# Kernel tuning notes

Hardware: AMD Instinct MI355X
Metric: run time of the kernel (lower is better)

The kernel has to match this reference:

```python
import jax, jax.numpy as jnp
import numpy as np

N_NODES = 50000
N_EDGES = 600000
D = 128


def setup_inputs() -> dict:
    key = jax.random.key(0)
    k1, k2, k3, k4 = jax.random.split(key, 4)
    x = jax.random.normal(k1, (N_NODES, D), dtype=jnp.float32)
    edge_index = jax.random.randint(k2, (2, N_EDGES), 0, N_NODES, dtype=jnp.int64)
    # GCNConv linear weight (glorot-ish scale) and bias
    W = jax.random.normal(k3, (D, D), dtype=jnp.float32) * (1.0 / np.sqrt(D))
    b = jax.random.normal(k4, (D,), dtype=jnp.float32) * 0.01
    return {"x": x, "edge_index": edge_index, "W": W, "b": b}


def reference(x, edge_index, W, b):
    """ResGCN: x + GCNConv(x, edge_index).

    GCNConv (PyG defaults): add self-loops, symmetric deg^{-1/2} normalization,
    messages x_j @ W scattered to destination nodes edge_index[1], plus bias.
    """
    n = x.shape[0]
    loop = jnp.arange(n, dtype=edge_index.dtype)
    src = jnp.concatenate([edge_index[0], loop])  # [E+N]
    dst = jnp.concatenate([edge_index[1], loop])  # [E+N]

    # degree on destination nodes (includes self-loops, edge_weight = 1)
    deg = jax.ops.segment_sum(jnp.ones(src.shape[0], x.dtype), dst, num_segments=n)
    deg_inv_sqrt = jnp.where(deg > 0, jax.lax.rsqrt(deg), jnp.zeros_like(deg))
    norm = deg_inv_sqrt[src] * deg_inv_sqrt[dst]  # [E+N]

    xw = x @ W  # [N, D] transform once, gather after
    msg = xw[src] * norm[:, None]  # [E+N, D]
    agg = jax.ops.segment_sum(msg, dst, num_segments=n)  # [N, D]
    res = agg + b
    return x + res
```

## Files before the change

kernel.cpp:

```cpp
#include <hip/hip_runtime.h>
#include <cstdint>

#define DD  128
#define CAP 32
#define SEB 2048
#define PAIRCAP 65536

typedef __attribute__((ext_vector_type(8))) short bf16x8;
typedef __attribute__((ext_vector_type(8))) unsigned short ushort8_t;
typedef __attribute__((ext_vector_type(4))) float f32x4;
typedef __attribute__((ext_vector_type(2))) float f32x2;

__device__ __forceinline__ short f2bf(float f) {
    union { float f; unsigned u; } v; v.f = f;
    unsigned r = v.u + 0x7FFFu + ((v.u >> 16) & 1u);
    return (short)(r >> 16);
}
__device__ __forceinline__ float bf2f(unsigned short s) {
    union { unsigned u; float f; } v; v.u = ((unsigned)s) << 16;
    return v.f;
}
__device__ __forceinline__ int load_idx(const void* ei, int flag, long long pos) {
    if (flag) return ((const int*)ei)[pos];
    return (int)((const long long*)ei)[pos];
}

__global__ __launch_bounds__(256) void prep_kernel(int4* __restrict__ zbase, int nz4,
                                                   const float* __restrict__ W,
                                                   short* __restrict__ Wp,
                                                   const void* ei, int E,
                                                   int* __restrict__ flag) {
    const int i = blockIdx.x * 256 + threadIdx.x;
    if (i < nz4) zbase[i] = make_int4(0, 0, 0, 0);
    if (i < DD * DD) {
        const int k = i >> 7, n = i & 127;
        Wp[n * DD + k] = f2bf(W[i]);
    }
    if (blockIdx.x == 0) {
        __shared__ int s_flag;
        if (threadIdx.x == 0) s_flag = 0;
        __syncthreads();
        const int n = E < 256 ? E : 256;
        if (threadIdx.x < n) {
            long long v = ((const long long*)ei)[threadIdx.x];
            if (v < 0 || v >= (1LL << 32)) atomicOr(&s_flag, 1);
        }
        __syncthreads();
        if (threadIdx.x == 0) *flag = s_flag;
    }
}

__device__ __forceinline__ void gemm_tile(const float* __restrict__ x,
                                          const short* __restrict__ Wp,
                                          short* __restrict__ xw,
                                          unsigned char* __restrict__ xwq,
                                          int N, int tile, int tid) {
    const int wave = tid >> 6;
    const int lane = tid & 63;
    const int lmod = lane & 15;
    const int lgrp = lane >> 4;
    const int rowbase = tile * 64 + wave * 16;
    const int arow = rowbase + lmod;
    const bool aok = arow < N;

    f32x4 acc[8];
#pragma unroll
    for (int i = 0; i < 8; ++i) acc[i] = (f32x4){0.f, 0.f, 0.f, 0.f};

#pragma unroll
    for (int ks = 0; ks < 4; ++ks) {
        const int kbase = ks * 32 + lgrp * 8;
        bf16x8 afrag;
        if (aok) {
            const float4 a0 = *(const float4*)&x[(size_t)arow * DD + kbase];
            const float4 a1 = *(const float4*)&x[(size_t)arow * DD + kbase + 4];
            afrag[0] = f2bf(a0.x); afrag[1] = f2bf(a0.y);
            afrag[2] = f2bf(a0.z); afrag[3] = f2bf(a0.w);
            afrag[4] = f2bf(a1.x); afrag[5] = f2bf(a1.y);
            afrag[6] = f2bf(a1.z); afrag[7] = f2bf(a1.w);
        } else {
#pragma unroll
            for (int i = 0; i < 8; ++i) afrag[i] = 0;
        }
#pragma unroll
        for (int nt = 0; nt < 8; ++nt) {
            bf16x8 bfrag = *(const bf16x8*)&Wp[(nt * 16 + lmod) * DD + kbase];
            acc[nt] = __builtin_amdgcn_mfma_f32_16x16x32_bf16(afrag, bfrag, acc[nt], 0, 0, 0);
        }
    }

#pragma unroll
    for (int r = 0; r < 4; ++r) {
        const int row = rowbase + lgrp * 4 + r;
        if (row < N) {
#pragma unroll
            for (int nt = 0; nt < 8; ++nt) {
                const float v = acc[nt][r];
                xw[(size_t)row * DD + nt * 16 + lmod] = f2bf(v);
                const unsigned q = __builtin_amdgcn_cvt_pk_fp8_f32(v, v, 0, false);
                xwq[(size_t)row * DD + nt * 16 + lmod] = (unsigned char)(q & 0xFF);
            }
        }
    }
}

__global__ __launch_bounds__(256) void stage_gemm(const void* ei, int E, int N,
                                                  int SBLK, int pcap, int npart,
                                                  const int* __restrict__ flag,
                                                  int* __restrict__ part_cursor,
                                                  unsigned* __restrict__ staging,
                                                  int2* __restrict__ pair,
                                                  int* __restrict__ ov_cnt,
                                                  const float* __restrict__ x,
                                                  const short* __restrict__ Wp,
                                                  short* __restrict__ xw,
                                                  unsigned char* __restrict__ xwq) {
    if ((int)blockIdx.x < SBLK) {
        __shared__ unsigned epack[SEB];
        __shared__ int hist[256];
        __shared__ int curs[256];
        const int f = *flag;
        const int base_e = blockIdx.x * SEB;
        const int ne = min(SEB, E - base_e);

        for (int i = threadIdx.x; i < ne; i += 256) {
            const unsigned s = (unsigned)load_idx(ei, f, base_e + i);
            const unsigned t = (unsigned)load_idx(ei, f, (long long)E + base_e + i);
            epack[i] = (t << 16) | s;
        }
        hist[threadIdx.x] = 0;
        __syncthreads();
        for (int i = threadIdx.x; i < ne; i += 256)
            atomicAdd(&hist[epack[i] >> 24], 1);
        __syncthreads();
        if (threadIdx.x < npart && hist[threadIdx.x] > 0)
            curs[threadIdx.x] = atomicAdd(&part_cursor[threadIdx.x], hist[threadIdx.x]);
        __syncthreads();
        for (int i = threadIdx.x; i < ne; i += 256) {
            const unsigned u = epack[i];
            const int part = u >> 24;
            const int pos = atomicAdd(&curs[part], 1);
            if (pos < pcap) {
                staging[(size_t)part * pcap + pos] = u & 0x00FFFFFFu;
            } else {
                const int p = atomicAdd(ov_cnt, 1);
                pair[PAIRCAP - 1 - p] = make_int2((int)(u >> 16), (int)(u & 0xFFFFu));
            }
        }
        return;
    }
    gemm_tile(x, Wp, xw, xwq, N, blockIdx.x - SBLK, threadIdx.x);
}

__global__ __launch_bounds__(256) void bucket_kernel(const unsigned* __restrict__ staging,
                                                     const int* __restrict__ part_cursor,
                                                     int pcap, int N,
                                                     int2* __restrict__ pair,
                                                     const int* __restrict__ ov_cnt,
                                                     int* __restrict__ spill_cnt,
                                                     int* __restrict__ col,
                                                     int* __restrict__ cnt) {
    const int part = blockIdx.x;
    const int node0 = part << 8;
    __shared__ int lcnt[256];
    lcnt[threadIdx.x] = 0;
    __syncthreads();

    const int nst = min(part_cursor[part], pcap);
    for (int i = threadIdx.x; i < nst; i += 256) {
        const unsigned u = staging[(size_t)part * pcap + i];
        const int dstl = (u >> 16) & 0xFF;
        const int src  = (int)(u & 0xFFFFu);
        const int r = atomicAdd(&lcnt[dstl], 1);
        if (r < CAP) col[(node0 + dstl) * CAP + r] = src;
        else { const int p = atomicAdd(spill_cnt, 1); pair[p] = make_int2(node0 + dstl, src); }
    }
    const int oc = *ov_cnt;
    for (int i = threadIdx.x; i < oc; i += 256) {
        const int2 ts = pair[PAIRCAP - 1 - i];
        if ((ts.x >> 8) == part) {
            const int r = atomicAdd(&lcnt[ts.x & 255], 1);
            if (r < CAP) col[ts.x * CAP + r] = ts.y;
            else { const int p = atomicAdd(spill_cnt, 1); pair[p] = make_int2(ts.x, ts.y); }
        }
    }
    __syncthreads();
    const int node = node0 + threadIdx.x;
    if (node < N) cnt[node] = lcnt[threadIdx.x];
}

__global__ __launch_bounds__(256) void gather_kernel(const short* __restrict__ xw,
                                                     const unsigned char* __restrict__ xwq,
                                                     const float* __restrict__ x,
                                                     const float* __restrict__ b,
                                                     const int* __restrict__ cnt,
                                                     const int* __restrict__ col,
                                                     const int2* __restrict__ pair,
                                                     const int* __restrict__ spill_cnt,
                                                     float* __restrict__ out, int N) {
    const int node = blockIdx.x * 16 + (threadIdx.x >> 4);
    if (node >= N) return;
    const int l = threadIdx.x & 15;
    const ushort8_t* xw8 = (const ushort8_t*)xw;
    const uint2* xq2 = (const uint2*)xwq;

    const int deg = cnt[node];
    const int nbk = deg < CAP ? deg : CAP;
    const float d = rsqrtf((float)(deg + 1));

    const int2 ir = ((const int2*)col)[node * 16 + l];
    const int s0 = (2 * l     < nbk) ? ir.x : 0;
    const int s1 = (2 * l + 1 < nbk) ? ir.y : 0;
    const float dsa = rsqrtf((float)(cnt[s0] + 1));
    const float dsb = rsqrtf((float)(cnt[s1] + 1));

    float acc[8], ac2[8];
    const ushort8_t sv = xw8[(size_t)node * 16 + l];
#pragma unroll
    for (int e = 0; e < 8; ++e) { acc[e] = d * bf2f(sv[e]); ac2[e] = 0.f; }

    int j = 0;
    for (; j + 8 <= nbk; j += 8) {
        int   sj[8];
        float dj[8];
#pragma unroll
        for (int u = 0; u < 8; ++u) {
            sj[u] = __shfl((u & 1) ? s1 : s0, (j + u) >> 1, 16);
            dj[u] = __shfl((u & 1) ? dsb : dsa, (j + u) >> 1, 16);
        }
        uint2 v[8];
#pragma unroll
        for (int u = 0; u < 8; ++u) v[u] = xq2[(size_t)sj[u] * 16 + l];
#pragma unroll
        for (int u = 0; u < 8; ++u) {
            float* A = (u & 1) ? ac2 : acc;
            const f32x2 p0 = __builtin_amdgcn_cvt_pk_f32_fp8(v[u].x, false);
            const f32x2 p1 = __builtin_amdgcn_cvt_pk_f32_fp8(v[u].x, true);
            const f32x2 p2 = __builtin_amdgcn_cvt_pk_f32_fp8(v[u].y, false);
            const f32x2 p3 = __builtin_amdgcn_cvt_pk_f32_fp8(v[u].y, true);
            A[0] = fmaf(dj[u], p0[0], A[0]); A[1] = fmaf(dj[u], p0[1], A[1]);
            A[2] = fmaf(dj[u], p1[0], A[2]); A[3] = fmaf(dj[u], p1[1], A[3]);
            A[4] = fmaf(dj[u], p2[0], A[4]); A[5] = fmaf(dj[u], p2[1], A[5]);
            A[6] = fmaf(dj[u], p3[0], A[6]); A[7] = fmaf(dj[u], p3[1], A[7]);
        }
    }
    for (; j + 4 <= nbk; j += 4) {
        int   sj[4];
        float dj[4];
#pragma unroll
        for (int u = 0; u < 4; ++u) {
            sj[u] = __shfl((u & 1) ? s1 : s0, (j + u) >> 1, 16);
            dj[u] = __shfl((u & 1) ? dsb : dsa, (j + u) >> 1, 16);
        }
        uint2 v[4];
#pragma unroll
        for (int u = 0; u < 4; ++u) v[u] = xq2[(size_t)sj[u] * 16 + l];
#pragma unroll
        for (int u = 0; u < 4; ++u) {
            float* A = (u & 1) ? ac2 : acc;
            const f32x2 p0 = __builtin_amdgcn_cvt_pk_f32_fp8(v[u].x, false);
            const f32x2 p1 = __builtin_amdgcn_cvt_pk_f32_fp8(v[u].x, true);
            const f32x2 p2 = __builtin_amdgcn_cvt_pk_f32_fp8(v[u].y, false);
            const f32x2 p3 = __builtin_amdgcn_cvt_pk_f32_fp8(v[u].y, true);
            A[0] = fmaf(dj[u], p0[0], A[0]); A[1] = fmaf(dj[u], p0[1], A[1]);
            A[2] = fmaf(dj[u], p1[0], A[2]); A[3] = fmaf(dj[u], p1[1], A[3]);
            A[4] = fmaf(dj[u], p2[0], A[4]); A[5] = fmaf(dj[u], p2[1], A[5]);
            A[6] = fmaf(dj[u], p3[0], A[6]); A[7] = fmaf(dj[u], p3[1], A[7]);
        }
    }
    for (; j < nbk; ++j) {
        const int   sj = __shfl((j & 1) ? s1 : s0, j >> 1, 16);
        const float dj = __shfl((j & 1) ? dsb : dsa, j >> 1, 16);
        const uint2 v = xq2[(size_t)sj * 16 + l];
        const f32x2 p0 = __builtin_amdgcn_cvt_pk_f32_fp8(v.x, false);
        const f32x2 p1 = __builtin_amdgcn_cvt_pk_f32_fp8(v.x, true);
        const f32x2 p2 = __builtin_amdgcn_cvt_pk_f32_fp8(v.y, false);
        const f32x2 p3 = __builtin_amdgcn_cvt_pk_f32_fp8(v.y, true);
        acc[0] = fmaf(dj, p0[0], acc[0]); acc[1] = fmaf(dj, p0[1], acc[1]);
        acc[2] = fmaf(dj, p1[0], acc[2]); acc[3] = fmaf(dj, p1[1], acc[3]);
        acc[4] = fmaf(dj, p2[0], acc[4]); acc[5] = fmaf(dj, p2[1], acc[5]);
        acc[6] = fmaf(dj, p3[0], acc[6]); acc[7] = fmaf(dj, p3[1], acc[7]);
    }

    if (deg > CAP) {
        const int sc = *spill_cnt;
        for (int i = 0; i < sc; ++i) {
            const int2 ts = pair[i];
            if (ts.x == node) {
                const float dss = rsqrtf((float)(cnt[ts.y] + 1));
                const ushort8_t v = xw8[(size_t)ts.y * 16 + l];
#pragma unroll
                for (int e = 0; e < 8; ++e) acc[e] = fmaf(dss, bf2f(v[e]), acc[e]);
            }
        }
    }

    const float4 x0 = *(const float4*)&x[(size_t)node * DD + l * 8];
    const float4 x1 = *(const float4*)&x[(size_t)node * DD + l * 8 + 4];
    const float4 b0 = *(const float4*)&b[l * 8];
    const float4 b1 = *(const float4*)&b[l * 8 + 4];
    float4 o0, o1;
    o0.x = x0.x + b0.x + d * (acc[0] + ac2[0]);
    o0.y = x0.y + b0.y + d * (acc[1] + ac2[1]);
    o0.z = x0.z + b0.z + d * (acc[2] + ac2[2]);
    o0.w = x0.w + b0.w + d * (acc[3] + ac2[3]);
    o1.x = x1.x + b1.x + d * (acc[4] + ac2[4]);
    o1.y = x1.y + b1.y + d * (acc[5] + ac2[5]);
    o1.z = x1.z + b1.z + d * (acc[6] + ac2[6]);
    o1.w = x1.w + b1.w + d * (acc[7] + ac2[7]);
    *(float4*)&out[(size_t)node * DD + l * 8]     = o0;
    *(float4*)&out[(size_t)node * DD + l * 8 + 4] = o1;
}

extern "C" void kernel_launch(void* const* d_in, const int* in_sizes, int n_in,
                              void* d_out, int out_size, void* d_ws, size_t ws_size,
                              hipStream_t stream) {
    const float* x  = (const float*)d_in[0];
    const void*  ei = d_in[1];
    const float* W  = (const float*)d_in[2];
    const float* b  = (const float*)d_in[3];
    float* out = (float*)d_out;

    const int N = in_sizes[0] / DD;
    const int E = in_sizes[1] / 2;

    const int npart = (N + 255) >> 8;
    const int pcap  = (((E / npart) * 7) / 5 + 512 + 255) & ~255;

    char* ws = (char*)d_ws;
    int*  spill_cnt   = (int*)ws;
    int*  ov_cnt      = (int*)(ws + 4);
    int*  flag        = (int*)(ws + 8);
    int*  part_cursor = (int*)(ws + 256);
    size_t off = 256 + (((size_t)npart * 4 + 255) & ~(size_t)255);
    int*  cnt = (int*)(ws + off);
    off += (size_t)N * 4;
    int*  col = (int*)(ws + off);
    off += (size_t)N * CAP * 4;
    unsigned* staging = (unsigned*)(ws + off);
    off += (size_t)npart * pcap * 4;
    off = (off + 255) & ~(size_t)255;
    int2* pair = (int2*)(ws + off);
    off += (size_t)PAIRCAP * 8;
    short* Wp = (short*)(ws + off);
    off += (size_t)DD * DD * 2;
    short* xw = (short*)(ws + off);
    off += (size_t)N * DD * 2;
    unsigned char* xwq = (unsigned char*)(ws + off);

    const int nz4 = (int)((256 + (size_t)npart * 4 + 15) / 16);
    const int pb  = ((nz4 > DD * DD ? nz4 : DD * DD) + 255) / 256;
    prep_kernel<<<pb, 256, 0, stream>>>((int4*)ws, nz4, W, Wp, ei, E, flag);

    const int SBLK = (E + SEB - 1) / SEB;
    const int GB   = (N + 63) / 64;
    stage_gemm<<<SBLK + GB, 256, 0, stream>>>(ei, E, N, SBLK, pcap, npart, flag,
                                              part_cursor, staging, pair, ov_cnt,
                                              x, Wp, xw, xwq);
    bucket_kernel<<<npart, 256, 0, stream>>>(staging, part_cursor, pcap, N,
                                             pair, ov_cnt, spill_cnt, col, cnt);
    gather_kernel<<<(N + 15) / 16, 256, 0, stream>>>(xw, xwq, x, b, cnt, col, pair,
                                                     spill_cnt, out, N);
}
```

Baseline: 69.54 us.

## Replace global-atomic partition staging with per-block sorted segments and drop prep kernel

Removes the prep kernel by having each staging block detect the index width itself and each GEMM block convert W to bf16 in shared memory. The staging blocks now locally sort their edges by partition, using a shared-memory prefix scan, and write per-block histograms and offsets. The bucket kernel reads those segments directly, which replaces the global part_cursor atomics and the staging overflow path. Overflow handling moves to a per-partition overflow area, with a fallback that rescans all segments. This saves one launch and the global contention, but every GEMM block now redoes the W conversion and the bucket kernel walks segments serially per block.

```diff
diff --git a/kernel.cpp b/kernel.cpp
--- a/kernel.cpp
+++ b/kernel.cpp
@@ -4,7 +4,7 @@
 #define DD  128
 #define CAP 32
 #define SEB 2048
-#define PAIRCAP 65536
+#define OVC 1024
 
 typedef __attribute__((ext_vector_type(8))) short bf16x8;
 typedef __attribute__((ext_vector_type(8))) unsigned short ushort8_t;
@@ -25,36 +25,87 @@
     return (int)((const long long*)ei)[pos];
 }
 
-__global__ __launch_bounds__(256) void prep_kernel(int4* __restrict__ zbase, int nz4,
-                                                   const float* __restrict__ W,
-                                                   short* __restrict__ Wp,
-                                                   const void* ei, int E,
-                                                   int* __restrict__ flag) {
-    const int i = blockIdx.x * 256 + threadIdx.x;
-    if (i < nz4) zbase[i] = make_int4(0, 0, 0, 0);
-    if (i < DD * DD) {
-        const int k = i >> 7, n = i & 127;
-        Wp[n * DD + k] = f2bf(W[i]);
-    }
-    if (blockIdx.x == 0) {
-        __shared__ int s_flag;
-        if (threadIdx.x == 0) s_flag = 0;
-        __syncthreads();
-        const int n = E < 256 ? E : 256;
-        if (threadIdx.x < n) {
-            long long v = ((const long long*)ei)[threadIdx.x];
-            if (v < 0 || v >= (1LL << 32)) atomicOr(&s_flag, 1);
-        }
-        __syncthreads();
-        if (threadIdx.x == 0) *flag = s_flag;
-    }
-}
-
-__device__ __forceinline__ void gemm_tile(const float* __restrict__ x,
-                                          const short* __restrict__ Wp,
-                                          short* __restrict__ xw,
-                                          unsigned char* __restrict__ xwq,
-                                          int N, int tile, int tid) {
+__global__ __launch_bounds__(256) void stage_gemm(const void* ei, int E, int N,
+                                                  int SBLK,
+                                                  unsigned* __restrict__ seg,
+                                                  int* __restrict__ blkhist,
+                                                  int* __restrict__ blkoff,
+                                                  const float* __restrict__ W,
+                                                  const float* __restrict__ x,
+                                                  short* __restrict__ xw,
+                                                  unsigned char* __restrict__ xwq) {
+    union SMem {
+        struct {
+            unsigned epack[SEB];
+            unsigned sorted[SEB];
+            int hist[256];
+            int scan[256];
+            int curs[256];
+            int flag;
+        } st;
+        short wp[DD * 136];
+    };
+    __shared__ SMem sm;
+    const int tid = threadIdx.x;
+    const int bid = blockIdx.x;
+
+    if (bid < SBLK) {
+        if (tid == 0) sm.st.flag = 0;
+        __syncthreads();
+        {
+            const int n = E < 256 ? E : 256;
+            if (tid < n) {
+                const long long v = ((const long long*)ei)[tid];
+                if (v < 0 || v >= (1LL << 32)) atomicOr(&sm.st.flag, 1);
+            }
+        }
+        __syncthreads();
+        const int f = sm.st.flag;
+        const int base_e = bid * SEB;
+        const int ne = min(SEB, E - base_e);
+
+        for (int i = tid; i < ne; i += 256) {
+            const unsigned s = (unsigned)load_idx(ei, f, base_e + i);
+            const unsigned t = (unsigned)load_idx(ei, f, (long long)E + base_e + i);
+            sm.st.epack[i] = (t << 16) | s;
+        }
+        sm.st.hist[tid] = 0;
+        __syncthreads();
+        for (int i = tid; i < ne; i += 256)
+            atomicAdd(&sm.st.hist[sm.st.epack[i] >> 24], 1);
+        __syncthreads();
+        const int hval = sm.st.hist[tid];
+        blkhist[bid * 256 + tid] = hval;
+        sm.st.scan[tid] = hval;
+        __syncthreads();
+        for (int off = 1; off < 256; off <<= 1) {
+            const int v = (tid >= off) ? sm.st.scan[tid - off] : 0;
+            __syncthreads();
+            sm.st.scan[tid] += v;
+            __syncthreads();
+        }
+        const int boff = sm.st.scan[tid] - hval;
+        blkoff[bid * 256 + tid] = boff;
+        sm.st.curs[tid] = boff;
+        __syncthreads();
+        for (int i = tid; i < ne; i += 256) {
+            const unsigned u = sm.st.epack[i];
+            const int pos = atomicAdd(&sm.st.curs[u >> 24], 1);
+            sm.st.sorted[pos] = u & 0x00FFFFFFu;
+        }
+        __syncthreads();
+        for (int i = tid; i < ne; i += 256)
+            seg[(size_t)bid * SEB + i] = sm.st.sorted[i];
+        return;
+    }
+
+    for (int e = tid; e < DD * DD; e += 256) {
+        const int k = e >> 7, n = e & 127;
+        sm.wp[n * 136 + k] = f2bf(W[e]);
+    }
+    __syncthreads();
+
+    const int tile = bid - SBLK;
     const int wave = tid >> 6;
     const int lane = tid & 63;
     const int lmod = lane & 15;
@@ -84,7 +135,7 @@
         }
 #pragma unroll
         for (int nt = 0; nt < 8; ++nt) {
-            bf16x8 bfrag = *(const bf16x8*)&Wp[(nt * 16 + lmod) * DD + kbase];
+            const bf16x8 bfrag = *(const bf16x8*)&sm.wp[(nt * 16 + lmod) * 136 + kbase];
             acc[nt] = __builtin_amdgcn_mfma_f32_16x16x32_bf16(afrag, bfrag, acc[nt], 0, 0, 0);
         }
     }
@@ -104,89 +155,41 @@
     }
 }
 
-__global__ __launch_bounds__(256) void stage_gemm(const void* ei, int E, int N,
-                                                  int SBLK, int pcap, int npart,
-                                                  const int* __restrict__ flag,
-                                                  int* __restrict__ part_cursor,
-                                                  unsigned* __restrict__ staging,
-                                                  int2* __restrict__ pair,
-                                                  int* __restrict__ ov_cnt,
-                                                  const float* __restrict__ x,
-                                                  const short* __restrict__ Wp,
-                                                  short* __restrict__ xw,
-                                                  unsigned char* __restrict__ xwq) {
-    if ((int)blockIdx.x < SBLK) {
-        __shared__ unsigned epack[SEB];
-        __shared__ int hist[256];
-        __shared__ int curs[256];
-        const int f = *flag;
-        const int base_e = blockIdx.x * SEB;
-        const int ne = min(SEB, E - base_e);
-
-        for (int i = threadIdx.x; i < ne; i += 256) {
-            const unsigned s = (unsigned)load_idx(ei, f, base_e + i);
-            const unsigned t = (unsigned)load_idx(ei, f, (long long)E + base_e + i);
-            epack[i] = (t << 16) | s;
-        }
-        hist[threadIdx.x] = 0;
-        __syncthreads();
-        for (int i = threadIdx.x; i < ne; i += 256)
-            atomicAdd(&hist[epack[i] >> 24], 1);
-        __syncthreads();
-        if (threadIdx.x < npart && hist[threadIdx.x] > 0)
-            curs[threadIdx.x] = atomicAdd(&part_cursor[threadIdx.x], hist[threadIdx.x]);
-        __syncthreads();
-        for (int i = threadIdx.x; i < ne; i += 256) {
-            const unsigned u = epack[i];
-            const int part = u >> 24;
-            const int pos = atomicAdd(&curs[part], 1);
-            if (pos < pcap) {
-                staging[(size_t)part * pcap + pos] = u & 0x00FFFFFFu;
-            } else {
-                const int p = atomicAdd(ov_cnt, 1);
-                pair[PAIRCAP - 1 - p] = make_int2((int)(u >> 16), (int)(u & 0xFFFFu));
-            }
-        }
-        return;
-    }
-    gemm_tile(x, Wp, xw, xwq, N, blockIdx.x - SBLK, threadIdx.x);
-}
-
-__global__ __launch_bounds__(256) void bucket_kernel(const unsigned* __restrict__ staging,
-                                                     const int* __restrict__ part_cursor,
-                                                     int pcap, int N,
-                                                     int2* __restrict__ pair,
-                                                     const int* __restrict__ ov_cnt,
-                                                     int* __restrict__ spill_cnt,
+__global__ __launch_bounds__(256) void bucket_kernel(const unsigned* __restrict__ seg,
+                                                     const int* __restrict__ blkhist,
+                                                     const int* __restrict__ blkoff,
+                                                     int SBLK, int N,
+                                                     unsigned* __restrict__ ovArea,
+                                                     int* __restrict__ ovcnt,
                                                      int* __restrict__ col,
                                                      int* __restrict__ cnt) {
     const int part = blockIdx.x;
     const int node0 = part << 8;
     __shared__ int lcnt[256];
+    __shared__ int lov;
     lcnt[threadIdx.x] = 0;
+    if (threadIdx.x == 0) lov = 0;
     __syncthreads();
 
-    const int nst = min(part_cursor[part], pcap);
-    for (int i = threadIdx.x; i < nst; i += 256) {
-        const unsigned u = staging[(size_t)part * pcap + i];
-        const int dstl = (u >> 16) & 0xFF;
-        const int src  = (int)(u & 0xFFFFu);
-        const int r = atomicAdd(&lcnt[dstl], 1);
-        if (r < CAP) col[(node0 + dstl) * CAP + r] = src;
-        else { const int p = atomicAdd(spill_cnt, 1); pair[p] = make_int2(node0 + dstl, src); }
-    }
-    const int oc = *ov_cnt;
-    for (int i = threadIdx.x; i < oc; i += 256) {
-        const int2 ts = pair[PAIRCAP - 1 - i];
-        if ((ts.x >> 8) == part) {
-            const int r = atomicAdd(&lcnt[ts.x & 255], 1);
-            if (r < CAP) col[ts.x * CAP + r] = ts.y;
-            else { const int p = atomicAdd(spill_cnt, 1); pair[p] = make_int2(ts.x, ts.y); }
+    for (int b = threadIdx.x; b < SBLK; b += 256) {
+        const int off = blkoff[b * 256 + part];
+        const int h   = blkhist[b * 256 + part];
+        const unsigned* s = &seg[(size_t)b * SEB + off];
+        for (int k = 0; k < h; ++k) {
+            const unsigned u = s[k];
+            const int dstl = (u >> 16) & 0xFF;
+            const int r = atomicAdd(&lcnt[dstl], 1);
+            if (r < CAP) col[(node0 + dstl) * CAP + r] = (int)(u & 0xFFFFu);
+            else {
+                const int o = atomicAdd(&lov, 1);
+                if (o < OVC) ovArea[part * OVC + o] = u;
+            }
         }
     }
     __syncthreads();
     const int node = node0 + threadIdx.x;
     if (node < N) cnt[node] = lcnt[threadIdx.x];
+    if (threadIdx.x == 0) ovcnt[part] = lov;
 }
 
 __global__ __launch_bounds__(256) void gather_kernel(const short* __restrict__ xw,
@@ -195,8 +198,12 @@
                                                      const float* __restrict__ b,
                                                      const int* __restrict__ cnt,
                                                      const int* __restrict__ col,
-                                                     const int2* __restrict__ pair,
-                                                     const int* __restrict__ spill_cnt,
+                                                     const unsigned* __restrict__ ovArea,
+                                                     const int* __restrict__ ovcnt,
+                                                     const unsigned* __restrict__ seg,
+                                                     const int* __restrict__ blkhist,
+                                                     const int* __restrict__ blkoff,
+                                                     int SBLK,
                                                      float* __restrict__ out, int N) {
     const int node = blockIdx.x * 16 + (threadIdx.x >> 4);
     if (node >= N) return;
@@ -207,6 +214,11 @@
     const int deg = cnt[node];
     const int nbk = deg < CAP ? deg : CAP;
     const float d = rsqrtf((float)(deg + 1));
+
+    const float4 x0 = *(const float4*)&x[(size_t)node * DD + l * 8];
+    const float4 x1 = *(const float4*)&x[(size_t)node * DD + l * 8 + 4];
+    const float4 b0 = *(const float4*)&b[l * 8];
+    const float4 b1 = *(const float4*)&b[l * 8 + 4];
 
     const int2 ir = ((const int2*)col)[node * 16 + l];
     const int s0 = (2 * l     < nbk) ? ir.x : 0;
@@ -283,22 +295,39 @@
     }
 
     if (deg > CAP) {
-        const int sc = *spill_cnt;
-        for (int i = 0; i < sc; ++i) {
-            const int2 ts = pair[i];
-            if (ts.x == node) {
-                const float dss = rsqrtf((float)(cnt[ts.y] + 1));
-                const ushort8_t v = xw8[(size_t)ts.y * 16 + l];
-#pragma unroll
-                for (int e = 0; e < 8; ++e) acc[e] = fmaf(dss, bf2f(v[e]), acc[e]);
-            }
-        }
-    }
-
-    const float4 x0 = *(const float4*)&x[(size_t)node * DD + l * 8];
-    const float4 x1 = *(const float4*)&x[(size_t)node * DD + l * 8 + 4];
-    const float4 b0 = *(const float4*)&b[l * 8];
-    const float4 b1 = *(const float4*)&b[l * 8 + 4];
+        const int part = node >> 8, dl = node & 255;
+        const int oc = ovcnt[part];
+        if (oc <= OVC) {
+            for (int i = 0; i < oc; ++i) {
+                const unsigned u = ovArea[part * OVC + i];
+                if ((int)((u >> 16) & 0xFF) == dl) {
+                    const int src = (int)(u & 0xFFFFu);
+                    const float dss = rsqrtf((float)(cnt[src] + 1));
+                    const ushort8_t v = xw8[(size_t)src * 16 + l];
+#pragma unroll
+                    for (int e = 0; e < 8; ++e) acc[e] = fmaf(dss, bf2f(v[e]), acc[e]);
+                }
+            }
+        } else {
+#pragma unroll
+            for (int e = 0; e < 8; ++e) { acc[e] = d * bf2f(sv[e]); ac2[e] = 0.f; }
+            for (int bb = 0; bb < SBLK; ++bb) {
+                const int off = blkoff[bb * 256 + part];
+                const int h   = blkhist[bb * 256 + part];
+                for (int k = 0; k < h; ++k) {
+                    const unsigned u = seg[(size_t)bb * SEB + off + k];
+                    if ((int)((u >> 16) & 0xFF) == dl) {
+                        const int src = (int)(u & 0xFFFFu);
+                        const float dss = rsqrtf((float)(cnt[src] + 1));
+                        const ushort8_t v = xw8[(size_t)src * 16 + l];
+#pragma unroll
+                        for (int e = 0; e < 8; ++e) acc[e] = fmaf(dss, bf2f(v[e]), acc[e]);
+                    }
+                }
+            }
+        }
+    }
+
     float4 o0, o1;
     o0.x = x0.x + b0.x + d * (acc[0] + ac2[0]);
     o0.y = x0.y + b0.y + d * (acc[1] + ac2[1]);
@@ -324,41 +353,28 @@
     const int N = in_sizes[0] / DD;
     const int E = in_sizes[1] / 2;
 
+    const int SBLK  = (E + SEB - 1) / SEB;
     const int npart = (N + 255) >> 8;
-    const int pcap  = (((E / npart) * 7) / 5 + 512 + 255) & ~255;
 
     char* ws = (char*)d_ws;
-    int*  spill_cnt   = (int*)ws;
-    int*  ov_cnt      = (int*)(ws + 4);
-    int*  flag        = (int*)(ws + 8);
-    int*  part_cursor = (int*)(ws + 256);
-    size_t off = 256 + (((size_t)npart * 4 + 255) & ~(size_t)255);
-    int*  cnt = (int*)(ws + off);
-    off += (size_t)N * 4;
-    int*  col = (int*)(ws + off);
-    off += (size_t)N * CAP * 4;
-    unsigned* staging = (unsigned*)(ws + off);
-    off += (size_t)npart * pcap * 4;
+    size_t off = 0;
+    unsigned* seg = (unsigned*)(ws + off);      off += (size_t)SBLK * SEB * 4;
+    int* blkhist  = (int*)(ws + off);           off += (size_t)SBLK * 256 * 4;
+    int* blkoff   = (int*)(ws + off);           off += (size_t)SBLK * 256 * 4;
+    int* cnt      = (int*)(ws + off);           off += (size_t)N * 4;
+    int* col      = (int*)(ws + off);           off += (size_t)N * CAP * 4;
+    int* ovcnt    = (int*)(ws + off);           off += 256 * 4;
+    unsigned* ovArea = (unsigned*)(ws + off);   off += (size_t)npart * OVC * 4;
     off = (off + 255) & ~(size_t)255;
-    int2* pair = (int2*)(ws + off);
-    off += (size_t)PAIRCAP * 8;
-    short* Wp = (short*)(ws + off);
-    off += (size_t)DD * DD * 2;
-    short* xw = (short*)(ws + off);
-    off += (size_t)N * DD * 2;
+    short* xw = (short*)(ws + off);             off += (size_t)N * DD * 2;
     unsigned char* xwq = (unsigned char*)(ws + off);
 
-    const int nz4 = (int)((256 + (size_t)npart * 4 + 15) / 16);
-    const int pb  = ((nz4 > DD * DD ? nz4 : DD * DD) + 255) / 256;
-    prep_kernel<<<pb, 256, 0, stream>>>((int4*)ws, nz4, W, Wp, ei, E, flag);
-
-    const int SBLK = (E + SEB - 1) / SEB;
-    const int GB   = (N + 63) / 64;
-    stage_gemm<<<SBLK + GB, 256, 0, stream>>>(ei, E, N, SBLK, pcap, npart, flag,
-                                              part_cursor, staging, pair, ov_cnt,
-                                              x, Wp, xw, xwq);
-    bucket_kernel<<<npart, 256, 0, stream>>>(staging, part_cursor, pcap, N,
-                                             pair, ov_cnt, spill_cnt, col, cnt);
-    gather_kernel<<<(N + 15) / 16, 256, 0, stream>>>(xw, xwq, x, b, cnt, col, pair,
-                                                     spill_cnt, out, N);
-}
+    const int GB = (N + 63) / 64;
+    stage_gemm<<<SBLK + GB, 256, 0, stream>>>(ei, E, N, SBLK, seg, blkhist, blkoff,
+                                              W, x, xw, xwq);
+    bucket_kernel<<<npart, 256, 0, stream>>>(seg, blkhist, blkoff, SBLK, N,
+                                             ovArea, ovcnt, col, cnt);
+    gather_kernel<<<(N + 15) / 16, 256, 0, stream>>>(xw, xwq, x, b, cnt, col,
+                                                     ovArea, ovcnt, seg, blkhist,
+                                                     blkoff, SBLK, out, N);
+}
```

Result: faster. 67.66 us (-2.7%).
